# Optimization experiments

Hardware: AMD Instinct MI355X
Metric: run time of the kernel (lower is better)

The kernel has to match this reference:

```python
import jax, jax.numpy as jnp
import numpy as np
from jax import lax

B_, H_, W_, C_ = 2, 64, 64, 96
DI, N_, R_, K_ = 192, 16, 6, 4  # d_inner=expand*C, d_state, dt_rank=ceil(96/16), 4 scan dirs


def _ln(x, g, b, eps):
    m = jnp.mean(x, axis=-1, keepdims=True)
    v = jnp.var(x, axis=-1, keepdims=True)
    return (x - m) / jnp.sqrt(v + eps) * g + b


def _conv1x1(x, w, b=None):
    y = jnp.einsum('bihw,oi->bohw', x, w)
    return y if b is None else y + b[None, :, None, None]


def _dwconv(x, w):
    return lax.conv_general_dilated(x, w, (1, 1), 'SAME',
                                    feature_group_count=x.shape[1],
                                    dimension_numbers=('NCHW', 'OIHW', 'NCHW'))


def _ss2d(x, in_proj_w, conv2d_w, conv2d_b, x_proj_w, dt_proj_w, dt_proj_b,
          A_logs, Ds, out_norm_g, out_norm_b, out_proj_w):
    B, H, W, C = x.shape
    L = H * W
    xz = jnp.einsum('bhwc,dc->bhwd', x, in_proj_w)          # [B,H,W,2*DI]
    xx, z = jnp.split(xz, 2, axis=-1)
    xc = jnp.transpose(xx, (0, 3, 1, 2))                    # [B,DI,H,W]
    xc = jax.nn.silu(_dwconv(xc, conv2d_w) + conv2d_b[None, :, None, None])
    # 4 scan directions: row-major, col-major, and their reverses
    x_hwwh = jnp.stack([xc.reshape(B, DI, L),
                        jnp.transpose(xc, (0, 1, 3, 2)).reshape(B, DI, L)], axis=1)
    xs = jnp.concatenate([x_hwwh, jnp.flip(x_hwwh, axis=-1)], axis=1)  # [B,K,DI,L]
    x_dbl = jnp.einsum('bkdl,kcd->bkcl', xs, x_proj_w)
    dts, Bs, Cs = jnp.split(x_dbl, [R_, R_ + N_], axis=2)   # [B,K,R,L],[B,K,N,L],[B,K,N,L]
    dt = jnp.einsum('bkrl,kdr->bkdl', dts, dt_proj_w) + dt_proj_b[None, :, :, None]
    dt = jax.nn.softplus(dt)
    A = -jnp.exp(A_logs).reshape(K_, DI, N_)

    def step(h, inp):
        u_t, dt_t, B_t, C_t = inp                            # [B,K,DI],[B,K,DI],[B,K,N],[B,K,N]
        dA = jnp.exp(dt_t[..., None] * A)                    # [B,K,DI,N]
        h = h * dA + (dt_t * u_t)[..., None] * B_t[:, :, None, :]
        y = jnp.einsum('bkdn,bkn->bkd', h, C_t)
        return h, y

    inps = (jnp.moveaxis(xs, -1, 0), jnp.moveaxis(dt, -1, 0),
            jnp.moveaxis(Bs, -1, 0), jnp.moveaxis(Cs, -1, 0))
    h0 = jnp.zeros((B, K_, DI, N_), xs.dtype)
    _, ys = lax.scan(step, h0, inps)                         # [L,B,K,DI]
    out_y = jnp.moveaxis(ys, 0, -1) + xs * Ds.reshape(K_, DI)[None, :, :, None]
    inv = jnp.flip(out_y[:, 2:4], axis=-1)
    y1 = out_y[:, 0]
    y2 = inv[:, 0]
    y3 = jnp.transpose(out_y[:, 1].reshape(B, DI, W, H), (0, 1, 3, 2)).reshape(B, DI, L)
    y4 = jnp.transpose(inv[:, 1].reshape(B, DI, W, H), (0, 1, 3, 2)).reshape(B, DI, L)
    y = jnp.transpose(y1 + y2 + y3 + y4, (0, 2, 1)).reshape(B, H, W, DI)
    y = _ln(y, out_norm_g, out_norm_b, 1e-5)
    y = y * jax.nn.silu(z)
    return jnp.einsum('bhwd,cd->bhwc', y, out_proj_w)


def _fftm(x, f1_w, f1_b, fm_w, fm_b, f2_w, f2_b):
    x = jax.nn.silu(_conv1x1(x, f1_w, f1_b))                 # [B,C/2,H,W]
    f = jnp.fft.rfftn(x, axes=(-2, -1), norm='ortho')        # [B,C/2,H,W//2+1] complex
    B, Ch, Hh, Wf = f.shape
    fr = jnp.stack([f.real, f.imag], axis=2).reshape(B, 2 * Ch, Hh, Wf)
    fr = jax.nn.silu(_conv1x1(fr, fm_w, fm_b))
    fr = fr.reshape(B, Ch, 2, Hh, Wf)
    fc = lax.complex(fr[:, :, 0], fr[:, :, 1])
    out = jnp.fft.irfftn(fc, s=x.shape[-2:], axes=(-2, -1), norm='ortho')
    return _conv1x1(out, f2_w, f2_b)


def _mgcb(x, in_w, dw3_w, dw5_w, out_w, ca_w1, ca_b1, ca_w2, ca_b2):
    Hd = 2 * x.shape[1]                                      # hidden_features = 2*dim
    p = _conv1x1(x, in_w)                                    # [B,2*Hd,H,W]
    s1 = 3 * Hd // 2
    x1, x2 = p[:, :s1], p[:, s1:]
    d1 = _dwconv(x1, dw3_w)
    x1_1, x1_2 = d1[:, :Hd], d1[:, Hd:]
    x2 = _dwconv(x2, dw5_w)
    y = jax.nn.gelu(x1_1, approximate=False) * jnp.concatenate([x1_2, x2], axis=1)
    y = _conv1x1(y, out_w)
    a = jnp.mean(y, axis=(2, 3))                             # channel attention (squeeze 30)
    a = jax.nn.relu(a @ ca_w1.T + ca_b1)
    a = jax.nn.sigmoid(a @ ca_w2.T + ca_b2)
    return y * a[:, :, None, None]


def _forward(input, ln1_g, ln1_b, skip_scale, skip_scale2, ln2_g, ln2_b,
             in_proj_w, conv2d_w, conv2d_b, x_proj_w, dt_proj_w, dt_proj_b,
             A_logs, Ds, out_norm_g, out_norm_b, out_proj_w,
             f1_w, f1_b, fm_w, fm_b, f2_w, f2_b,
             mg_in_w, mg_dw3_w, mg_dw5_w, mg_out_w,
             ca_w1, ca_b1, ca_w2, ca_b2, h_size, w_size):
    B, L, C = input.shape
    x4 = input.reshape(B, h_size, w_size, C)
    xn = _ln(x4, ln1_g, ln1_b, 1e-6)
    attn = _ss2d(xn, in_proj_w, conv2d_w, conv2d_b, x_proj_w, dt_proj_w,
                 dt_proj_b, A_logs, Ds, out_norm_g, out_norm_b, out_proj_w)
    fft = _fftm(jnp.transpose(xn, (0, 3, 1, 2)), f1_w, f1_b, fm_w, fm_b, f2_w, f2_b)
    x = x4 * skip_scale + attn + jnp.transpose(fft, (0, 2, 3, 1))
    xn2 = _ln(x, ln2_g, ln2_b, 1e-5)
    conv = _mgcb(jnp.transpose(xn2, (0, 3, 1, 2)), mg_in_w, mg_dw3_w, mg_dw5_w,
                 mg_out_w, ca_w1, ca_b1, ca_w2, ca_b2)
    x = x * skip_scale2 + jnp.transpose(conv, (0, 2, 3, 1))
    return x.reshape(B, L, C)


def setup_inputs() -> dict:
    key = jax.random.key(0)
    ks = iter(jax.random.split(key, 48))
    def rn(shape, s=0.02):
        return jax.random.normal(next(ks), shape, jnp.float32) * s
    d = {}
    d['input'] = jax.random.normal(next(ks), (B_, H_ * W_, C_), jnp.float32)
    d['ln1_g'] = jnp.ones((C_,)); d['ln1_b'] = jnp.zeros((C_,))
    d['skip_scale'] = jnp.ones((C_,)); d['skip_scale2'] = jnp.ones((C_,))
    d['ln2_g'] = jnp.ones((C_,)); d['ln2_b'] = jnp.zeros((C_,))
    d['in_proj_w'] = rn((2 * DI, C_))
    d['conv2d_w'] = rn((DI, 1, 3, 3), 0.1); d['conv2d_b'] = jnp.zeros((DI,))
    d['x_proj_w'] = rn((K_, R_ + 2 * N_, DI))
    d['dt_proj_w'] = rn((K_, DI, R_), 0.1)
    d['dt_proj_b'] = jnp.full((K_, DI), -4.6, jnp.float32) + rn((K_, DI), 0.5)
    d['A_logs'] = jnp.log(jnp.tile(jnp.arange(1, N_ + 1, dtype=jnp.float32), (K_ * DI, 1)))
    d['Ds'] = jnp.ones((K_ * DI,))
    d['out_norm_g'] = jnp.ones((DI,)); d['out_norm_b'] = jnp.zeros((DI,))
    d['out_proj_w'] = rn((C_, DI))
    Ch = C_ // 2
    d['f1_w'] = rn((Ch, C_)); d['f1_b'] = jnp.zeros((Ch,))
    d['fm_w'] = rn((C_, C_)); d['fm_b'] = jnp.zeros((C_,))
    d['f2_w'] = rn((C_, Ch)); d['f2_b'] = jnp.zeros((C_,))
    Hd = 2 * C_
    d['mg_in_w'] = rn((2 * Hd, C_))
    d['mg_dw3_w'] = rn((3 * Hd // 2, 1, 3, 3), 0.1)
    d['mg_dw5_w'] = rn((Hd // 2, 1, 5, 5), 0.1)
    d['mg_out_w'] = rn((C_, Hd))
    Csq = C_ // 30
    d['ca_w1'] = rn((Csq, C_)); d['ca_b1'] = jnp.zeros((Csq,))
    d['ca_w2'] = rn((C_, Csq)); d['ca_b2'] = jnp.zeros((C_,))
    d['h_size'] = H_
    d['w_size'] = W_
    return d


def reference(input, ln1_g, ln1_b, skip_scale, skip_scale2, ln2_g, ln2_b,
              in_proj_w, conv2d_w, conv2d_b, x_proj_w, dt_proj_w, dt_proj_b,
              A_logs, Ds, out_norm_g, out_norm_b, out_proj_w,
              f1_w, f1_b, fm_w, fm_b, f2_w, f2_b,
              mg_in_w, mg_dw3_w, mg_dw5_w, mg_out_w,
              ca_w1, ca_b1, ca_w2, ca_b2, h_size, w_size):
    return _forward(input, ln1_g, ln1_b, skip_scale, skip_scale2, ln2_g, ln2_b,
                    in_proj_w, conv2d_w, conv2d_b, x_proj_w, dt_proj_w, dt_proj_b,
                    A_logs, Ds, out_norm_g, out_norm_b, out_proj_w,
                    f1_w, f1_b, fm_w, fm_b, f2_w, f2_b,
                    mg_in_w, mg_dw3_w, mg_dw5_w, mg_out_w,
                    ca_w1, ca_b1, ca_w2, ca_b2, h_size, w_size)
```

## Files before the change

kernel.cpp:

```cpp
#include <hip/hip_runtime.h>
#include <math.h>

#define DEV __device__ __forceinline__

constexpr int DI = 192, Nn = 16, Rr = 6;
constexpr int Cc = 96;
constexpr int Ll = 4096;
constexpr int NC = 64;

DEV float silu_(float x) { return x / (1.f + __expf(-x)); }
DEV float qadd1(float v) {
  int i = __builtin_amdgcn_mov_dpp(__float_as_int(v), 0xB1, 0xF, 0xF, true);
  return v + __int_as_float(i);
}
DEV float qadd2(float v) {
  int i = __builtin_amdgcn_mov_dpp(__float_as_int(v), 0x4E, 0xF, 0xF, true);
  return v + __int_as_float(i);
}

template<int CIN, int COUT, int CB, int PXB, int IN_MODE, int OUT_MODE, int ACT, int HAS_BIAS, int LN>
__global__ void conv1x1v2_kernel(const float* __restrict__ in, const float4* __restrict__ wt,
                                 const float* __restrict__ bias, float* __restrict__ out,
                                 float* __restrict__ out2, const float* __restrict__ lng,
                                 const float* __restrict__ lnb) {
  constexpr int J4 = CIN / 4, STR = J4 + 1, CCN = CB / 16, PXT = PXB / 16;
  constexpr int NPB = 8192 / PXB;
  __shared__ float4 xv[PXB * STR];
  int t = threadIdx.x;
  int pb = blockIdx.x % NPB;
  int cbase = (blockIdx.x / NPB) * CB;
  int pbase = pb * PXB;
  if (IN_MODE == 0) {
    for (int idx = t; idx < PXB * J4; idx += 256) {
      int px = idx / J4, j4 = idx - px * J4;
      xv[px * STR + j4] = ((const float4*)in)[(size_t)(pbase + px) * J4 + j4];
    }
  } else {
    for (int idx = t; idx < PXB * CIN; idx += 256) {
      int px = idx & (PXB - 1), c = idx / PXB;
      int gp = pbase + px; int b = gp >> 12, p = gp & 4095;
      ((float*)xv)[px * (STR * 4) + c] = in[((size_t)b * CIN + c) * Ll + p];
    }
  }
  __syncthreads();
  if constexpr (LN) {
    constexpr int TPX = 256 / PXB;
    constexpr int CHUNK = CIN / TPX;
    int px = t / TPX, sub = t % TPX;
    float* row = (float*)(xv + px * STR);
    float sm = 0.f, sq = 0.f;
    #pragma unroll
    for (int j2 = 0; j2 < CHUNK; ++j2) {
      float v = row[sub + j2 * TPX];
      sm += v; sq += v * v;
    }
    #pragma unroll
    for (int m = 1; m < TPX; m <<= 1) {
      sm += __shfl_xor(sm, m, 64);
      sq += __shfl_xor(sq, m, 64);
    }
    float mean = sm * (1.f / CIN);
    float rs = rsqrtf(sq * (1.f / CIN) - mean * mean + 1e-6f);
    #pragma unroll
    for (int j2 = 0; j2 < CHUNK; ++j2) {
      int j = sub + j2 * TPX;
      row[j] = (row[j] - mean) * rs * lng[j] + lnb[j];
    }
    __syncthreads();
  }
  int g = t >> 4, ci = t & 15;
  float acc[PXT][CCN];
  #pragma unroll
  for (int cc = 0; cc < CCN; ++cc) {
    float b0 = HAS_BIAS ? bias[cbase + ci + 16 * cc] : 0.f;
    #pragma unroll
    for (int p = 0; p < PXT; ++p) acc[p][cc] = b0;
  }
  #pragma unroll 2
  for (int j4 = 0; j4 < J4; ++j4) {
    float4 xr[PXT];
    #pragma unroll
    for (int p = 0; p < PXT; ++p) xr[p] = xv[(g + 16 * p) * STR + j4];
    #pragma unroll
    for (int cc = 0; cc < CCN; ++cc) {
      float4 w4 = wt[(size_t)j4 * COUT + cbase + ci + 16 * cc];
      #pragma unroll
      for (int p = 0; p < PXT; ++p)
        acc[p][cc] += xr[p].x * w4.x + xr[p].y * w4.y + xr[p].z * w4.z + xr[p].w * w4.w;
    }
  }
  #pragma unroll
  for (int p = 0; p < PXT; ++p) {
    int gp = pbase + g + 16 * p;
    #pragma unroll
    for (int cc = 0; cc < CCN; ++cc) {
      int c = cbase + ci + 16 * cc;
      float v = acc[p][cc];
      if (OUT_MODE == 2) {
        if (c < 192) out[(size_t)gp * 192 + c] = v;
        else out2[(size_t)gp * 192 + (c - 192)] = silu_(v);
      } else {
        if (ACT == 1) v = silu_(v);
        if (OUT_MODE == 0) out[(size_t)gp * COUT + c] = v;
        else { int bb = gp >> 12, p2 = gp & 4095; out[((size_t)bb * COUT + c) * Ll + p2] = v; }
      }
    }
  }
}

__global__ void outproj_fused_kernel(
    const float* __restrict__ outy, const float* __restrict__ zs,
    const float* __restrict__ ong, const float* __restrict__ onb,
    const float4* __restrict__ wt, const float* __restrict__ input,
    const float* __restrict__ fftout, const float* __restrict__ ss,
    const float* __restrict__ ln2g, const float* __restrict__ ln2b,
    float* __restrict__ xres, float* __restrict__ xn2) {
  __shared__ float4 xv[32 * 49];
  int t = threadIdx.x;
  int pbase = blockIdx.x * 32;
  {
    int px = t >> 3, sub = t & 7;
    int pix = pbase + px;
    int p = pix & 4095, b = pix >> 12;
    int pt = ((p & 63) << 6) | (p >> 6);
    size_t base = (size_t)b * 4 * Ll * DI;
    const float* y0 = outy + base + (size_t)p * DI;
    const float* y1 = outy + base + ((size_t)Ll + pt) * DI;
    const float* y2 = outy + base + ((size_t)2 * Ll + (4095 - p)) * DI;
    const float* y3 = outy + base + ((size_t)3 * Ll + (4095 - pt)) * DI;
    float v[24];
    float sm = 0.f, sq = 0.f;
    #pragma unroll
    for (int j = 0; j < 24; ++j) {
      int c = sub + 8 * j;
      float vv = y0[c] + y1[c] + y2[c] + y3[c];
      v[j] = vv; sm += vv; sq += vv * vv;
    }
    #pragma unroll
    for (int m = 1; m < 8; m <<= 1) {
      sm += __shfl_xor(sm, m, 64);
      sq += __shfl_xor(sq, m, 64);
    }
    float mean = sm * (1.f / 192.f);
    float rs = rsqrtf(sq * (1.f / 192.f) - mean * mean + 1e-5f);
    const float* zrow = zs + (size_t)pix * DI;
    float* row = (float*)(xv + px * 49);
    #pragma unroll
    for (int j = 0; j < 24; ++j) {
      int c = sub + 8 * j;
      row[c] = ((v[j] - mean) * rs * ong[c] + onb[c]) * zrow[c];
    }
  }
  __syncthreads();
  int g = t >> 4, ci = t & 15;
  float acc[2][6];
  #pragma unroll
  for (int pI = 0; pI < 2; ++pI)
    #pragma unroll
    for (int cc = 0; cc < 6; ++cc) acc[pI][cc] = 0.f;
  #pragma unroll 2
  for (int j4 = 0; j4 < 48; ++j4) {
    float4 xr0 = xv[g * 49 + j4];
    float4 xr1 = xv[(g + 16) * 49 + j4];
    #pragma unroll
    for (int cc = 0; cc < 6; ++cc) {
      float4 w4 = wt[(size_t)j4 * 96 + ci + 16 * cc];
      acc[0][cc] += xr0.x * w4.x + xr0.y * w4.y + xr0.z * w4.z + xr0.w * w4.w;
      acc[1][cc] += xr1.x * w4.x + xr1.y * w4.y + xr1.z * w4.z + xr1.w * w4.w;
    }
  }
  #pragma unroll
  for (int pI = 0; pI < 2; ++pI) {
    int gp = pbase + g + 16 * pI;
    float vv[6];
    float sm = 0.f, sq = 0.f;
    #pragma unroll
    for (int cc = 0; cc < 6; ++cc) {
      int c = ci + 16 * cc;
      float x = input[(size_t)gp * Cc + c] * ss[c] + acc[pI][cc] + fftout[(size_t)gp * Cc + c];
      vv[cc] = x; sm += x; sq += x * x;
    }
    #pragma unroll
    for (int m = 1; m < 16; m <<= 1) {
      sm += __shfl_xor(sm, m, 64);
      sq += __shfl_xor(sq, m, 64);
    }
    float mean = sm * (1.f / 96.f);
    float rs = rsqrtf(sq * (1.f / 96.f) - mean * mean + 1e-5f);
    #pragma unroll
    for (int cc = 0; cc < 6; ++cc) {
      int c = ci + 16 * cc;
      xres[(size_t)gp * Cc + c] = vv[cc];
      xn2[(size_t)gp * Cc + c] = (vv[cc] - mean) * rs * ln2g[c] + ln2b[c];
    }
  }
}

__global__ void mgout_fused_kernel(const float* __restrict__ in, const float4* __restrict__ wt,
                                   float* __restrict__ out, float* __restrict__ cap) {
  __shared__ float4 xv[32 * 49];
  __shared__ float redc[4][96];
  int t = threadIdx.x;
  int pbase = blockIdx.x * 32;
  for (int idx = t; idx < 32 * 48; idx += 256) {
    int px = idx / 48, j4 = idx - px * 48;
    xv[px * 49 + j4] = ((const float4*)in)[(size_t)(pbase + px) * 48 + j4];
  }
  __syncthreads();
  int g = t >> 4, ci = t & 15;
  float acc[2][6];
  #pragma unroll
  for (int pI = 0; pI < 2; ++pI)
    #pragma unroll
    for (int cc = 0; cc < 6; ++cc) acc[pI][cc] = 0.f;
  #pragma unroll 2
  for (int j4 = 0; j4 < 48; ++j4) {
    float4 xr0 = xv[g * 49 + j4];
    float4 xr1 = xv[(g + 16) * 49 + j4];
    #pragma unroll
    for (int cc = 0; cc < 6; ++cc) {
      float4 w4 = wt[(size_t)j4 * 96 + ci + 16 * cc];
      acc[0][cc] += xr0.x * w4.x + xr0.y * w4.y + xr0.z * w4.z + xr0.w * w4.w;
      acc[1][cc] += xr1.x * w4.x + xr1.y * w4.y + xr1.z * w4.z + xr1.w * w4.w;
    }
  }
  float ps[6];
  #pragma unroll
  for (int cc = 0; cc < 6; ++cc) ps[cc] = acc[0][cc] + acc[1][cc];
  #pragma unroll
  for (int pI = 0; pI < 2; ++pI) {
    int gp = pbase + g + 16 * pI;
    #pragma unroll
    for (int cc = 0; cc < 6; ++cc)
      out[(size_t)gp * 96 + ci + 16 * cc] = acc[pI][cc];
  }
  #pragma unroll
  for (int cc = 0; cc < 6; ++cc) {
    ps[cc] += __shfl_xor(ps[cc], 16, 64);
    ps[cc] += __shfl_xor(ps[cc], 32, 64);
  }
  if ((t & 63) < 16) {
    #pragma unroll
    for (int cc = 0; cc < 6; ++cc) redc[t >> 6][ci + 16 * cc] = ps[cc];
  }
  __syncthreads();
  if (t < 96)
    cap[(size_t)blockIdx.x * 96 + t] = redc[0][t] + redc[1][t] + redc[2][t] + redc[3][t];
}

__global__ void camerge_kernel(const float* __restrict__ cap, const float* __restrict__ w1,
                               const float* __restrict__ b1, const float* __restrict__ w2,
                               const float* __restrict__ b2, float* __restrict__ avec) {
  __shared__ float red[4][192];
  __shared__ float means[192];
  int t = threadIdx.x;
  int q = t / 192, r = t % 192;
  int b = r / 96, c = r % 96;
  float s = 0.f;
  for (int j = 0; j < 32; ++j)
    s += cap[(size_t)(b * 128 + q * 32 + j) * 96 + c];
  red[q][r] = s;
  __syncthreads();
  if (t < 192)
    means[t] = (red[0][t] + red[1][t] + red[2][t] + red[3][t]) * (1.f / 4096.f);
  __syncthreads();
  if (t < 192) {
    int bb = t / 96, cc2 = t % 96;
    float tt[3];
    #pragma unroll
    for (int j = 0; j < 3; ++j) {
      float a = b1[j];
      for (int cc = 0; cc < 96; ++cc) a += means[bb * 96 + cc] * w1[j * 96 + cc];
      tt[j] = fmaxf(a, 0.f);
    }
    float a2 = b2[cc2];
    #pragma unroll
    for (int j = 0; j < 3; ++j) a2 += tt[j] * w2[cc2 * 3 + j];
    avec[t] = 1.f / (1.f + expf(-a2));
  }
}

__global__ void wprep_all_kernel(const float* __restrict__ xpw, float4* __restrict__ xpwT,
                                 const float* __restrict__ cw, const float* __restrict__ mg3,
                                 const float* __restrict__ mg5, float* __restrict__ WC3T,
                                 float* __restrict__ W3T, float* __restrict__ W5T,
                                 const float* __restrict__ ipw, float4* __restrict__ WIPT,
                                 const float* __restrict__ mgiw, float4* __restrict__ WMGT,
                                 const float* __restrict__ opw, float4* __restrict__ WOPT,
                                 const float* __restrict__ mgow, float4* __restrict__ WMOT,
                                 const float* __restrict__ f1w, float4* __restrict__ WF1T,
                                 const float* __restrict__ f2w, float4* __restrict__ WF2T) {
  int idx = blockIdx.x * 256 + threadIdx.x;
  if (idx < 9216) {
    int k = idx / (48 * 48);
    int r = idx % (48 * 48);
    int j4 = r / 48, c = r % 48;
    float4 v = make_float4(0.f, 0.f, 0.f, 0.f);
    if (c < 38) v = ((const float4*)xpw)[((size_t)k * 38 + c) * 48 + j4];
    xpwT[((size_t)k * 48 + j4) * 48 + c] = v;
  }
  if (idx < 1728) { int c = idx / 9, j = idx % 9; WC3T[j * 192 + c] = cw[idx]; }
  if (idx < 2592) { int c = idx / 9, j = idx % 9; W3T[j * 288 + c] = mg3[idx]; }
  if (idx < 2400) { int c = idx / 25, j = idx % 25; W5T[j * 96 + c] = mg5[idx]; }
  if (idx < 9216) { int oc = idx % 384, j4 = idx / 384; WIPT[idx] = ((const float4*)ipw)[(size_t)oc * 24 + j4]; }
  if (idx < 9216) { int oc = idx % 384, j4 = idx / 384; WMGT[idx] = ((const float4*)mgiw)[(size_t)oc * 24 + j4]; }
  if (idx < 4608) { int oc = idx % 96, j4 = idx / 96; WOPT[idx] = ((const float4*)opw)[(size_t)oc * 48 + j4]; }
  if (idx < 4608) { int oc = idx % 96, j4 = idx / 96; WMOT[idx] = ((const float4*)mgow)[(size_t)oc * 48 + j4]; }
  if (idx < 1152) { int oc = idx % 48, j4 = idx / 48; WF1T[idx] = ((const float4*)f1w)[(size_t)oc * 24 + j4]; }
  if (idx < 1152) { int oc = idx % 96, j4 = idx / 96; WF2T[idx] = ((const float4*)f2w)[(size_t)oc * 12 + j4]; }
}

__global__ void dwconv3_silu_kernel(const float* __restrict__ xx, const float* __restrict__ wc3t,
                                    const float* __restrict__ bias, float* __restrict__ xc,
                                    float* __restrict__ xct) {
  int idx = blockIdx.x * 256 + threadIdx.x;
  int d4 = idx % 48;
  int p = (idx / 48) & (Ll - 1);
  int b = idx / (48 * Ll);
  int h = p >> 6, wq = p & 63;
  const float4* base = (const float4*)xx + (size_t)b * Ll * 48;
  const float4* wt = (const float4*)wc3t;
  float4 bv = ((const float4*)bias)[d4];
  float a0 = bv.x, a1 = bv.y, a2 = bv.z, a3 = bv.w;
  #pragma unroll
  for (int i = 0; i < 3; ++i) {
    int hh = h - 1 + i;
    if ((unsigned)hh >= 64u) continue;
    #pragma unroll
    for (int j = 0; j < 3; ++j) {
      int ww2 = wq - 1 + j;
      if ((unsigned)ww2 >= 64u) continue;
      float4 x = base[(size_t)(hh * 64 + ww2) * 48 + d4];
      float4 w4 = wt[(i * 3 + j) * 48 + d4];
      a0 += x.x * w4.x; a1 += x.y * w4.y; a2 += x.z * w4.z; a3 += x.w * w4.w;
    }
  }
  float4 v = make_float4(silu_(a0), silu_(a1), silu_(a2), silu_(a3));
  ((float4*)xc)[idx] = v;
  int pt = (wq << 6) | h;
  ((float4*)xct)[((size_t)b * Ll + pt) * 48 + d4] = v;
}

__global__ void proj_kernel(const float* __restrict__ xc, const float4* __restrict__ xpwT,
                            float* __restrict__ BSo, float* __restrict__ CSo,
                            float* __restrict__ DTS) {
  __shared__ float4 xv[32 * 49];
  int t = threadIdx.x;
  int pb = blockIdx.x & 127;
  int k = (blockIdx.x >> 7) & 3;
  int b = blockIdx.x >> 9;
  int bk = b * 4 + k;
  int pbase = pb * 32;
  for (int idx = t; idx < 32 * 48; idx += 256) {
    int it = idx / 48, j4 = idx - it * 48;
    xv[it * 49 + j4] = ((const float4*)xc)[((size_t)b * Ll + pbase + it) * 48 + j4];
  }
  __syncthreads();
  int g = t >> 4, ci = t & 15;
  float acc[2][3];
  #pragma unroll
  for (int p = 0; p < 2; ++p)
    #pragma unroll
    for (int cc = 0; cc < 3; ++cc) acc[p][cc] = 0.f;
  #pragma unroll 2
  for (int j4 = 0; j4 < 48; ++j4) {
    float4 xr0 = xv[g * 49 + j4];
    float4 xr1 = xv[(g + 16) * 49 + j4];
    const float4* wrow = xpwT + ((size_t)k * 48 + j4) * 48;
    #pragma unroll
    for (int cc = 0; cc < 3; ++cc) {
      float4 w4 = wrow[ci + 16 * cc];
      acc[0][cc] += xr0.x * w4.x + xr0.y * w4.y + xr0.z * w4.z + xr0.w * w4.w;
      acc[1][cc] += xr1.x * w4.x + xr1.y * w4.y + xr1.z * w4.z + xr1.w * w4.w;
    }
  }
  #pragma unroll
  for (int pI = 0; pI < 2; ++pI) {
    int p = pbase + g + 16 * pI;
    int pt = ((p & 63) << 6) | (p >> 6);
    int l = (k == 0) ? p : (k == 1) ? pt : (k == 2) ? (4095 - p) : (4095 - pt);
    #pragma unroll
    for (int cc = 0; cc < 3; ++cc) {
      int c = ci + 16 * cc;
      float v = acc[pI][cc];
      if (c < 6) DTS[((size_t)bk * 6 + c) * Ll + l] = v;
      else if (c < 22) BSo[((size_t)bk * Ll + l) * Nn + (c - 6)] = v;
      else if (c < 38) CSo[((size_t)bk * Ll + l) * Nn + (c - 22)] = v;
    }
  }
}

__global__ void dtproj_kernel(const float* __restrict__ dts, const float* __restrict__ dtw,
                              const float* __restrict__ dtb, float* __restrict__ DTo) {
  __shared__ float sdts[6][64];
  int t = threadIdx.x;
  int lb = (blockIdx.x & 63) * 64;
  int bk = blockIdx.x >> 6;
  int k = bk & 3;
  if (t < 384) {
    int r = t / 64, l = t & 63;
    sdts[r][l] = dts[((size_t)bk * 6 + r) * Ll + lb + l];
  }
  __syncthreads();
  int d = t;
  const float* wr = dtw + ((size_t)k * DI + d) * Rr;
  float w0 = wr[0], w1 = wr[1], w2 = wr[2], w3 = wr[3], w4 = wr[4], w5 = wr[5];
  float b0 = dtb[k * DI + d];
  float* ob = DTo + ((size_t)bk * Ll + lb) * DI + d;
  #pragma unroll 4
  for (int l = 0; l < 64; ++l) {
    float a = b0 + sdts[0][l] * w0 + sdts[1][l] * w1 + sdts[2][l] * w2
            + sdts[3][l] * w3 + sdts[4][l] * w4 + sdts[5][l] * w5;
    float sp = (a > 20.f) ? a : log1pf(__expf(a));
    ob[(size_t)l * DI] = sp;
  }
}

__global__ void scanA_kernel(const float* __restrict__ dtg, const float* __restrict__ xc,
                             const float* __restrict__ xct, const float* __restrict__ bsg,
                             const float* __restrict__ alog,
                             float* __restrict__ P, float* __restrict__ Q) {
  int g = blockIdx.x * 256 + threadIdx.x;
  int ng = g & 3;
  int t1 = g >> 2;
  int d = t1 % DI;
  int t2 = t1 / DI;
  int c = t2 & 63;
  int bk = t2 >> 6;
  int k = bk & 3, b = bk >> 2;
  float4 al = ((const float4*)alog)[(size_t)(k * DI + d) * 4 + ng];
  float An0 = -__expf(al.x), An1 = -__expf(al.y), An2 = -__expf(al.z), An3 = -__expf(al.w);
  const float* dtp = dtg + ((size_t)bk * Ll + c * 64) * DI + d;
  const float4* bsp = (const float4*)bsg + ((size_t)bk * Ll + c * 64) * 4 + ng;
  const float* usrc = (k & 1) ? xct : xc;
  int p0 = (k >= 2) ? (4095 - c * 64) : (c * 64);
  int ustep = (k >= 2) ? -DI : DI;
  const float* up = usrc + ((size_t)b * Ll + p0) * DI + d;
  float P0 = 1.f, P1 = 1.f, P2 = 1.f, P3 = 1.f;
  float Q0 = 0.f, Q1 = 0.f, Q2 = 0.f, Q3 = 0.f;
  float dpre[4], upre[4];
  float4 bpre[4];
  #pragma unroll
  for (int i = 0; i < 4; ++i) {
    dpre[i] = dtp[(size_t)i * DI];
    upre[i] = up[(ptrdiff_t)i * ustep];
    bpre[i] = bsp[(size_t)i * 4];
  }
  for (int tg = 0; tg < 64; tg += 4) {
    #pragma unroll
    for (int i = 0; i < 4; ++i) {
      float dtv = dpre[i], u = upre[i];
      float4 Bv = bpre[i];
      int tn = tg + 4 + i;
      dpre[i] = dtp[(size_t)tn * DI];
      upre[i] = up[(ptrdiff_t)tn * ustep];
      bpre[i] = bsp[(size_t)tn * 4];
      float s = dtv * u;
      float a0 = __expf(dtv * An0), a1 = __expf(dtv * An1);
      float a2 = __expf(dtv * An2), a3 = __expf(dtv * An3);
      P0 *= a0; P1 *= a1; P2 *= a2; P3 *= a3;
      Q0 = Q0 * a0 + s * Bv.x; Q1 = Q1 * a1 + s * Bv.y;
      Q2 = Q2 * a2 + s * Bv.z; Q3 = Q3 * a3 + s * Bv.w;
    }
  }
  ((float4*)P)[g] = make_float4(P0, P1, P2, P3);
  ((float4*)Q)[g] = make_float4(Q0, Q1, Q2, Q3);
}

__global__ void scanB_kernel(const float* __restrict__ P, const float* __restrict__ Q,
                             float* __restrict__ H0) {
  int g = blockIdx.x * 256 + threadIdx.x;
  int n = g & 15;
  int d = (g >> 4) % DI;
  int bk = (g >> 4) / DI;
  size_t base = (size_t)bk * NC * DI * Nn + (size_t)d * Nn + n;
  float Ppre[4], Qpre[4];
  #pragma unroll
  for (int i = 0; i < 4; ++i) {
    Ppre[i] = P[base + (size_t)i * 3072];
    Qpre[i] = Q[base + (size_t)i * 3072];
  }
  float h = 0.f;
  for (int cg = 0; cg < 64; cg += 4) {
    #pragma unroll
    for (int i = 0; i < 4; ++i) {
      float pv = Ppre[i], qv = Qpre[i];
      Ppre[i] = P[base + (size_t)(cg + 4 + i) * 3072];
      Qpre[i] = Q[base + (size_t)(cg + 4 + i) * 3072];
      H0[base + (size_t)(cg + i) * 3072] = h;
      h = pv * h + qv;
    }
  }
}

__global__ void scanC_kernel(const float* __restrict__ dtg, const float* __restrict__ xc,
                             const float* __restrict__ xct, const float* __restrict__ bsg,
                             const float* __restrict__ csg, const float* __restrict__ alog,
                             const float* __restrict__ Dsv_, const float* __restrict__ H0,
                             float* __restrict__ outy) {
  int g = blockIdx.x * 256 + threadIdx.x;
  int ng = g & 3;
  int t1 = g >> 2;
  int d = t1 % DI;
  int t2 = t1 / DI;
  int c = t2 & 63;
  int bk = t2 >> 6;
  int k = bk & 3, b = bk >> 2;
  float4 al = ((const float4*)alog)[(size_t)(k * DI + d) * 4 + ng];
  float An0 = -__expf(al.x), An1 = -__expf(al.y), An2 = -__expf(al.z), An3 = -__expf(al.w);
  float Dsv = Dsv_[k * DI + d];
  const float* dtp = dtg + ((size_t)bk * Ll + c * 64) * DI + d;
  const float4* bsp = (const float4*)bsg + ((size_t)bk * Ll + c * 64) * 4 + ng;
  const float4* csp = (const float4*)csg + ((size_t)bk * Ll + c * 64) * 4 + ng;
  const float* usrc = (k & 1) ? xct : xc;
  int p0 = (k >= 2) ? (4095 - c * 64) : (c * 64);
  int ustep = (k >= 2) ? -DI : DI;
  const float* up = usrc + ((size_t)b * Ll + p0) * DI + d;
  float* yo = outy + ((size_t)bk * Ll + c * 64) * DI + d;
  float4 h4 = ((const float4*)H0)[g];
  float h0 = h4.x, h1 = h4.y, h2 = h4.z, h3 = h4.w;
  float dpre[4], upre[4];
  float4 bpre[4], cpre[4];
  #pragma unroll
  for (int i = 0; i < 4; ++i) {
    dpre[i] = dtp[(size_t)i * DI];
    upre[i] = up[(ptrdiff_t)i * ustep];
    bpre[i] = bsp[(size_t)i * 4];
    cpre[i] = csp[(size_t)i * 4];
  }
  for (int tg = 0; tg < 64; tg += 4) {
    #pragma unroll
    for (int i = 0; i < 4; ++i) {
      float dtv = dpre[i], u = upre[i];
      float4 Bv = bpre[i], Cv = cpre[i];
      int tn = tg + 4 + i;
      dpre[i] = dtp[(size_t)tn * DI];
      upre[i] = up[(ptrdiff_t)tn * ustep];
      bpre[i] = bsp[(size_t)tn * 4];
      cpre[i] = csp[(size_t)tn * 4];
      float s = dtv * u;
      float a0 = __expf(dtv * An0), a1 = __expf(dtv * An1);
      float a2 = __expf(dtv * An2), a3 = __expf(dtv * An3);
      h0 = h0 * a0 + s * Bv.x; h1 = h1 * a1 + s * Bv.y;
      h2 = h2 * a2 + s * Bv.z; h3 = h3 * a3 + s * Bv.w;
      float yp = h0 * Cv.x + h1 * Cv.y + h2 * Cv.z + h3 * Cv.w;
      yp = qadd1(yp);
      yp = qadd2(yp);
      if (ng == 0) yo[(size_t)(tg + i) * DI] = yp + u * Dsv;
    }
  }
}

__global__ void dft_row_kernel(const float* __restrict__ xf, float* __restrict__ Tr,
                               float* __restrict__ Ti) {
  __shared__ float row[4][64];
  __shared__ float cs[64], sn[64];
  int t = threadIdx.x, lane = t & 63, wv = t >> 6;
  int bch = blockIdx.x * 4 + wv;
  int h = bch & 63, bc = bch >> 6;
  row[wv][lane] = xf[(size_t)bch * 64 + lane];
  if (t < 64) {
    float ang = (float)t * 0.09817477042468103f;
    float s0, c0; sincosf(ang, &s0, &c0); sn[t] = s0; cs[t] = c0;
  }
  __syncthreads();
  if (lane < 33) {
    float ar = 0.f, ai = 0.f;
    for (int wq = 0; wq < 64; ++wq) {
      int j = (lane * wq) & 63;
      ar += row[wv][wq] * cs[j];
      ai -= row[wv][wq] * sn[j];
    }
    Tr[((size_t)bc * 33 + lane) * 64 + h] = ar;
    Ti[((size_t)bc * 33 + lane) * 64 + h] = ai;
  }
}

__global__ void dft_col_kernel(const float* __restrict__ Tr, const float* __restrict__ Ti,
                               float* __restrict__ Gr, float* __restrict__ Gi) {
  __shared__ float tr[4][64], ti[4][64];
  __shared__ float cs[64], sn[64];
  int t = threadIdx.x, lane = t & 63, wv = t >> 6;
  int idx = blockIdx.x * 4 + wv;
  int v = idx % 33, bc = idx / 33;
  tr[wv][lane] = Tr[((size_t)bc * 33 + v) * 64 + lane];
  ti[wv][lane] = Ti[((size_t)bc * 33 + v) * 64 + lane];
  if (t < 64) {
    float ang = (float)t * 0.09817477042468103f;
    float s0, c0; sincosf(ang, &s0, &c0); sn[t] = s0; cs[t] = c0;
  }
  __syncthreads();
  float ar = 0.f, ai = 0.f;
  for (int hh = 0; hh < 64; ++hh) {
    int j = (lane * hh) & 63;
    ar += tr[wv][hh] * cs[j] + ti[wv][hh] * sn[j];
    ai += ti[wv][hh] * cs[j] - tr[wv][hh] * sn[j];
  }
  Gr[((size_t)bc * 64 + lane) * 33 + v] = ar * (1.f / 64.f);
  Gi[((size_t)bc * 64 + lane) * 33 + v] = ai * (1.f / 64.f);
}

__global__ void fmix2_kernel(const float* __restrict__ Gr, const float* __restrict__ Gi,
                             const float* __restrict__ w, const float* __restrict__ bias,
                             float* __restrict__ Mr, float* __restrict__ Mi) {
  __shared__ float xs[16][100];
  int t = threadIdx.x;
  int uvb = (blockIdx.x % 132) * 16;
  int b = blockIdx.x / 132;
  for (int idx = t; idx < 96 * 16; idx += 256) {
    int ch = idx >> 4, px = idx & 15;
    const float* src = (ch & 1) ? Gi : Gr;
    xs[px][ch] = src[((size_t)(b * 48 + (ch >> 1))) * 2112 + uvb + px];
  }
  __syncthreads();
  int px = t >> 4, ci = t & 15;
  float acc[6];
  #pragma unroll
  for (int cc = 0; cc < 6; ++cc) acc[cc] = bias[ci + 16 * cc];
  const float4* xr4 = (const float4*)&xs[px][0];
  #pragma unroll 2
  for (int j4 = 0; j4 < 24; ++j4) {
    float4 x4 = xr4[j4];
    #pragma unroll
    for (int cc = 0; cc < 6; ++cc) {
      float4 w4 = ((const float4*)w)[(size_t)(ci + 16 * cc) * 24 + j4];
      acc[cc] += x4.x * w4.x + x4.y * w4.y + x4.z * w4.z + x4.w * w4.w;
    }
  }
  int uv = uvb + px;
  int u = uv / 33, vv2 = uv % 33;
  #pragma unroll
  for (int cc = 0; cc < 6; ++cc) {
    int o = ci + 16 * cc;
    float v = silu_(acc[cc]);
    float* dst = (o & 1) ? Mi : Mr;
    dst[((size_t)(b * 48 + (o >> 1))) * 2112 + vv2 * 64 + u] = v;
  }
}

__global__ void idft_col_kernel(const float* __restrict__ Mr, const float* __restrict__ Mi,
                                float* __restrict__ gr, float* __restrict__ gi) {
  __shared__ float mr[4][64], mi[4][64];
  __shared__ float cs[64], sn[64];
  int t = threadIdx.x, lane = t & 63, wv = t >> 6;
  int idx = blockIdx.x * 4 + wv;
  int v = idx % 33, bc = idx / 33;
  mr[wv][lane] = Mr[((size_t)bc * 33 + v) * 64 + lane];
  mi[wv][lane] = Mi[((size_t)bc * 33 + v) * 64 + lane];
  if (t < 64) {
    float ang = (float)t * 0.09817477042468103f;
    float s0, c0; sincosf(ang, &s0, &c0); sn[t] = s0; cs[t] = c0;
  }
  __syncthreads();
  float ar = 0.f, ai = 0.f;
  for (int u = 0; u < 64; ++u) {
    int j = (lane * u) & 63;
    ar += mr[wv][u] * cs[j] - mi[wv][u] * sn[j];
    ai += mr[wv][u] * sn[j] + mi[wv][u] * cs[j];
  }
  gr[((size_t)bc * 64 + lane) * 33 + v] = ar;
  gi[((size_t)bc * 64 + lane) * 33 + v] = ai;
}

__global__ void irfft_row_kernel(const float* __restrict__ gr, const float* __restrict__ gi,
                                 float* __restrict__ ysp) {
  __shared__ float r[4][33], im[4][33];
  __shared__ float cs[64], sn[64];
  int t = threadIdx.x, lane = t & 63, wv = t >> 6;
  int bch = blockIdx.x * 4 + wv;
  if (lane < 33) {
    r[wv][lane] = gr[(size_t)bch * 33 + lane];
    im[wv][lane] = gi[(size_t)bch * 33 + lane];
  }
  if (t < 64) {
    float ang = (float)t * 0.09817477042468103f;
    float s0, c0; sincosf(ang, &s0, &c0); sn[t] = s0; cs[t] = c0;
  }
  __syncthreads();
  float acc = r[wv][0] + ((lane & 1) ? -r[wv][32] : r[wv][32]);
  for (int v = 1; v < 32; ++v) {
    int j = (v * lane) & 63;
    acc += 2.f * (r[wv][v] * cs[j] - im[wv][v] * sn[j]);
  }
  ysp[(size_t)bch * 64 + lane] = acc * (1.f / 64.f);
}

__global__ void mgcb_dw_kernel(const float* __restrict__ pm, const float* __restrict__ w3t,
                               const float* __restrict__ w5t, float* __restrict__ ymg) {
  int idx = blockIdx.x * 256 + threadIdx.x;
  int c4 = idx % 48;
  int p = (idx / 48) & (Ll - 1);
  int b = idx / (48 * Ll);
  int h = p >> 6, wq = p & 63;
  const float4* base = (const float4*)pm + (size_t)b * Ll * 96;
  const float4* wt3 = (const float4*)w3t;
  float g0 = 0.f, g1 = 0.f, g2 = 0.f, g3 = 0.f;
  float m0 = 0.f, m1 = 0.f, m2 = 0.f, m3 = 0.f;
  if (c4 < 24) {
    #pragma unroll
    for (int i = 0; i < 3; ++i) {
      int hh = h - 1 + i; if ((unsigned)hh >= 64u) continue;
      #pragma unroll
      for (int j = 0; j < 3; ++j) {
        int ww2 = wq - 1 + j; if ((unsigned)ww2 >= 64u) continue;
        const float4* px = base + (size_t)(hh * 64 + ww2) * 96;
        float4 xg = px[c4];
        float4 wg = wt3[(i * 3 + j) * 72 + c4];
        g0 += xg.x * wg.x; g1 += xg.y * wg.y; g2 += xg.z * wg.z; g3 += xg.w * wg.w;
        float4 xm = px[48 + c4];
        float4 wm = wt3[(i * 3 + j) * 72 + 48 + c4];
        m0 += xm.x * wm.x; m1 += xm.y * wm.y; m2 += xm.z * wm.z; m3 += xm.w * wm.w;
      }
    }
  } else {
    #pragma unroll
    for (int i = 0; i < 3; ++i) {
      int hh = h - 1 + i; if ((unsigned)hh >= 64u) continue;
      #pragma unroll
      for (int j = 0; j < 3; ++j) {
        int ww2 = wq - 1 + j; if ((unsigned)ww2 >= 64u) continue;
        float4 xg = base[(size_t)(hh * 64 + ww2) * 96 + c4];
        float4 wg = wt3[(i * 3 + j) * 72 + c4];
        g0 += xg.x * wg.x; g1 += xg.y * wg.y; g2 += xg.z * wg.z; g3 += xg.w * wg.w;
      }
    }
    const float4* wt5 = (const float4*)w5t;
    int cw4 = c4 - 24;
    #pragma unroll
    for (int i = 0; i < 5; ++i) {
      int hh = h - 2 + i; if ((unsigned)hh >= 64u) continue;
      #pragma unroll
      for (int j = 0; j < 5; ++j) {
        int ww2 = wq - 2 + j; if ((unsigned)ww2 >= 64u) continue;
        float4 xm = base[(size_t)(hh * 64 + ww2) * 96 + 48 + c4];
        float4 wm = wt5[(i * 5 + j) * 24 + cw4];
        m0 += xm.x * wm.x; m1 += xm.y * wm.y; m2 += xm.z * wm.z; m3 += xm.w * wm.w;
      }
    }
  }
  const float IS2 = 0.70710678118654752f;
  float4 o;
  o.x = 0.5f * g0 * (1.f + erff(g0 * IS2)) * m0;
  o.y = 0.5f * g1 * (1.f + erff(g1 * IS2)) * m1;
  o.z = 0.5f * g2 * (1.f + erff(g2 * IS2)) * m2;
  o.w = 0.5f * g3 * (1.f + erff(g3 * IS2)) * m3;
  ((float4*)ymg)[idx] = o;
}

__global__ void final_kernel(const float* __restrict__ xres, const float* __restrict__ yc,
                             const float* __restrict__ ss2, const float* __restrict__ avec,
                             float* __restrict__ out) {
  int i4 = blockIdx.x * 256 + threadIdx.x;
  int e0 = i4 * 4;
  int c = e0 % 96;
  int b = e0 / (Ll * 96);
  float4 xr = ((const float4*)xres)[i4];
  float4 yv = ((const float4*)yc)[i4];
  const float* av = avec + b * 96 + c;
  const float* sv = ss2 + c;
  float4 o;
  o.x = xr.x * sv[0] + yv.x * av[0];
  o.y = xr.y * sv[1] + yv.y * av[1];
  o.z = xr.z * sv[2] + yv.z * av[2];
  o.w = xr.w * sv[3] + yv.w * av[3];
  ((float4*)out)[i4] = o;
}

extern "C" void kernel_launch(void* const* d_in, const int* in_sizes, int n_in,
                              void* d_out, int out_size, void* d_ws, size_t ws_size,
                              hipStream_t stream) {
  const float* input      = (const float*)d_in[0];
  const float* ln1_g      = (const float*)d_in[1];
  const float* ln1_b      = (const float*)d_in[2];
  const float* skip_scale = (const float*)d_in[3];
  const float* skip_scale2= (const float*)d_in[4];
  const float* ln2_g      = (const float*)d_in[5];
  const float* ln2_b      = (const float*)d_in[6];
  const float* in_proj_w  = (const float*)d_in[7];
  const float* conv2d_w   = (const float*)d_in[8];
  const float* conv2d_b   = (const float*)d_in[9];
  const float* x_proj_w   = (const float*)d_in[10];
  const float* dt_proj_w  = (const float*)d_in[11];
  const float* dt_proj_b  = (const float*)d_in[12];
  const float* A_logs     = (const float*)d_in[13];
  const float* Ds         = (const float*)d_in[14];
  const float* out_norm_g = (const float*)d_in[15];
  const float* out_norm_b = (const float*)d_in[16];
  const float* out_proj_w = (const float*)d_in[17];
  const float* f1_w       = (const float*)d_in[18];
  const float* f1_b       = (const float*)d_in[19];
  const float* fm_w       = (const float*)d_in[20];
  const float* fm_b       = (const float*)d_in[21];
  const float* f2_w       = (const float*)d_in[22];
  const float* f2_b       = (const float*)d_in[23];
  const float* mg_in_w    = (const float*)d_in[24];
  const float* mg_dw3_w   = (const float*)d_in[25];
  const float* mg_dw5_w   = (const float*)d_in[26];
  const float* mg_out_w   = (const float*)d_in[27];
  const float* ca_w1      = (const float*)d_in[28];
  const float* ca_b1      = (const float*)d_in[29];
  const float* ca_w2      = (const float*)d_in[30];
  const float* ca_b2      = (const float*)d_in[31];

  float* W = (float*)d_ws;
  float* XN    = W;
  float* ZSILU = XN + 786432;
  float* XX    = ZSILU + 1572864;
  float* XC    = XX + 1572864;
  float* XCT   = XC + 1572864;
  float* DT    = XCT + 1572864;
  float* BSb   = DT + 6291456;
  float* CSb   = BSb + 524288;
  float* PP    = CSb + 524288;
  float* QQ    = PP + 1572864;
  float* H0    = QQ + 1572864;
  float* OUTY  = H0 + 1572864;
  float* YGATE = OUTY + 6291456;
  float* ATTN  = YGATE + 1572864;
  float* FFTOUT= ATTN + 786432;
  float* XRES  = FFTOUT + 786432;
  float* XN2   = XRES + 786432;
  float* MEANS = XN2 + 786432;
  float* AVEC  = MEANS + 192;
  float* XPWT  = AVEC + 192;
  float* WC3T  = XPWT + 36864;
  float* W3T   = WC3T + 1728;
  float* W5T   = W3T + 2592;
  float* CAP   = W5T + 2400;
  float* WIPT  = CAP + 24576;
  float* WMGT  = WIPT + 36864;
  float* WOPT  = WMGT + 36864;
  float* WMOT  = WOPT + 18432;
  float* WF1T  = WMOT + 18432;
  float* WF2T  = WF1T + 4608;
  float* DTS = H0;
  float* XF  = PP;
  float* TR  = XF + 393216;
  float* TI  = TR + 202752;
  float* GR  = TI + 202752;
  float* GI  = GR + 202752;
  float* MR  = TR;
  float* MI  = TI;
  float* G2R = GR;
  float* G2I = GI;
  float* YSP = GI + 202752;
  float* PMG = DT;
  float* YMG = DT + 3145728;
  float* YCb = YMG + 1572864;

  wprep_all_kernel<<<36, 256, 0, stream>>>(
      x_proj_w, (float4*)XPWT, conv2d_w, mg_dw3_w, mg_dw5_w, WC3T, W3T, W5T,
      in_proj_w, (float4*)WIPT, mg_in_w, (float4*)WMGT, out_proj_w, (float4*)WOPT,
      mg_out_w, (float4*)WMOT, f1_w, (float4*)WF1T, f2_w, (float4*)WF2T);
  conv1x1v2_kernel<96, 384, 96, 64, 0, 2, 0, 0, 1><<<512, 256, 0, stream>>>(
      input, (const float4*)WIPT, nullptr, XX, ZSILU, ln1_g, ln1_b);
  dwconv3_silu_kernel<<<1536, 256, 0, stream>>>(XX, WC3T, conv2d_b, XC, XCT);
  proj_kernel<<<1024, 256, 0, stream>>>(XC, (const float4*)XPWT, BSb, CSb, DTS);
  dtproj_kernel<<<512, 192, 0, stream>>>(DTS, dt_proj_w, dt_proj_b, DT);
  scanA_kernel<<<1536, 256, 0, stream>>>(DT, XC, XCT, BSb, A_logs, PP, QQ);
  scanB_kernel<<<96, 256, 0, stream>>>(PP, QQ, H0);
  conv1x1v2_kernel<96, 48, 48, 32, 0, 1, 1, 1, 1><<<256, 256, 0, stream>>>(
      input, (const float4*)WF1T, f1_b, XF, nullptr, ln1_g, ln1_b);
  dft_row_kernel<<<1536, 256, 0, stream>>>(XF, TR, TI);
  dft_col_kernel<<<792, 256, 0, stream>>>(TR, TI, GR, GI);
  fmix2_kernel<<<264, 256, 0, stream>>>(GR, GI, fm_w, fm_b, MR, MI);
  idft_col_kernel<<<792, 256, 0, stream>>>(MR, MI, G2R, G2I);
  irfft_row_kernel<<<1536, 256, 0, stream>>>(G2R, G2I, YSP);
  conv1x1v2_kernel<48, 96, 96, 32, 1, 0, 0, 1, 0><<<256, 256, 0, stream>>>(
      YSP, (const float4*)WF2T, f2_b, FFTOUT, nullptr, nullptr, nullptr);
  scanC_kernel<<<1536, 256, 0, stream>>>(DT, XC, XCT, BSb, CSb, A_logs, Ds, H0, OUTY);
  outproj_fused_kernel<<<256, 256, 0, stream>>>(
      OUTY, ZSILU, out_norm_g, out_norm_b, (const float4*)WOPT, input, FFTOUT,
      skip_scale, ln2_g, ln2_b, XRES, XN2);
  conv1x1v2_kernel<96, 384, 96, 64, 0, 0, 0, 0, 0><<<512, 256, 0, stream>>>(
      XN2, (const float4*)WMGT, nullptr, PMG, nullptr, nullptr, nullptr);
  mgcb_dw_kernel<<<1536, 256, 0, stream>>>(PMG, W3T, W5T, YMG);
  mgout_fused_kernel<<<256, 256, 0, stream>>>(YMG, (const float4*)WMOT, YCb, CAP);
  camerge_kernel<<<1, 768, 0, stream>>>(CAP, ca_w1, ca_b1, ca_w2, ca_b2, AVEC);
  final_kernel<<<768, 256, 0, stream>>>(XRES, YCb, skip_scale2, AVEC, (float*)d_out);
}
```

Baseline: 346.5 us.

## Fuse row and column DFT passes into per-channel 2D DFT kernels

The separate row-DFT and column-DFT kernels, and likewise the inverse column and row kernels, are merged so that one block per (batch, channel) plane does both passes through shared memory. This drops the global intermediate arrays and two kernel launches. The cost is that each fused kernel launches only 96 blocks, which may leave most compute units idle, and each block now carries far more serial work per thread using a naive O(N^2) DFT.

```diff
diff --git a/kernel.cpp b/kernel.cpp
--- a/kernel.cpp
+++ b/kernel.cpp
@@ -551,53 +551,45 @@
   }
 }
 
-__global__ void dft_row_kernel(const float* __restrict__ xf, float* __restrict__ Tr,
-                               float* __restrict__ Ti) {
-  __shared__ float row[4][64];
+__global__ void dft2d_kernel(const float* __restrict__ xf, float* __restrict__ Gr,
+                             float* __restrict__ Gi) {
+  __shared__ float xs[64][65];
+  __shared__ float tr[33][65], ti[33][65];
   __shared__ float cs[64], sn[64];
-  int t = threadIdx.x, lane = t & 63, wv = t >> 6;
-  int bch = blockIdx.x * 4 + wv;
-  int h = bch & 63, bc = bch >> 6;
-  row[wv][lane] = xf[(size_t)bch * 64 + lane];
+  int t = threadIdx.x;
+  int bc = blockIdx.x;
+  const float* src = xf + (size_t)bc * 4096;
+  for (int i = t; i < 4096; i += 256) xs[i >> 6][i & 63] = src[i];
   if (t < 64) {
     float ang = (float)t * 0.09817477042468103f;
     float s0, c0; sincosf(ang, &s0, &c0); sn[t] = s0; cs[t] = c0;
   }
   __syncthreads();
-  if (lane < 33) {
+  for (int o = t; o < 33 * 64; o += 256) {
+    int v = o >> 6, h = o & 63;
     float ar = 0.f, ai = 0.f;
-    for (int wq = 0; wq < 64; ++wq) {
-      int j = (lane * wq) & 63;
-      ar += row[wv][wq] * cs[j];
-      ai -= row[wv][wq] * sn[j];
-    }
-    Tr[((size_t)bc * 33 + lane) * 64 + h] = ar;
-    Ti[((size_t)bc * 33 + lane) * 64 + h] = ai;
-  }
-}
-
-__global__ void dft_col_kernel(const float* __restrict__ Tr, const float* __restrict__ Ti,
-                               float* __restrict__ Gr, float* __restrict__ Gi) {
-  __shared__ float tr[4][64], ti[4][64];
-  __shared__ float cs[64], sn[64];
-  int t = threadIdx.x, lane = t & 63, wv = t >> 6;
-  int idx = blockIdx.x * 4 + wv;
-  int v = idx % 33, bc = idx / 33;
-  tr[wv][lane] = Tr[((size_t)bc * 33 + v) * 64 + lane];
-  ti[wv][lane] = Ti[((size_t)bc * 33 + v) * 64 + lane];
-  if (t < 64) {
-    float ang = (float)t * 0.09817477042468103f;
-    float s0, c0; sincosf(ang, &s0, &c0); sn[t] = s0; cs[t] = c0;
-  }
-  __syncthreads();
-  float ar = 0.f, ai = 0.f;
-  for (int hh = 0; hh < 64; ++hh) {
-    int j = (lane * hh) & 63;
-    ar += tr[wv][hh] * cs[j] + ti[wv][hh] * sn[j];
-    ai += ti[wv][hh] * cs[j] - tr[wv][hh] * sn[j];
-  }
-  Gr[((size_t)bc * 64 + lane) * 33 + v] = ar * (1.f / 64.f);
-  Gi[((size_t)bc * 64 + lane) * 33 + v] = ai * (1.f / 64.f);
+    for (int w = 0; w < 64; ++w) {
+      int j = (v * w) & 63;
+      float x = xs[h][w];
+      ar += x * cs[j];
+      ai -= x * sn[j];
+    }
+    tr[v][h] = ar; ti[v][h] = ai;
+  }
+  __syncthreads();
+  for (int o = t; o < 64 * 33; o += 256) {
+    int u = o / 33, v = o - u * 33;
+    float ar = 0.f, ai = 0.f;
+    for (int h = 0; h < 64; ++h) {
+      int j = (u * h) & 63;
+      float c = cs[j], s = sn[j];
+      float trv = tr[v][h], tiv = ti[v][h];
+      ar += trv * c + tiv * s;
+      ai += tiv * c - trv * s;
+    }
+    Gr[((size_t)bc * 64 + u) * 33 + v] = ar * (1.f / 64.f);
+    Gi[((size_t)bc * 64 + u) * 33 + v] = ai * (1.f / 64.f);
+  }
 }
 
 __global__ void fmix2_kernel(const float* __restrict__ Gr, const float* __restrict__ Gi,
@@ -638,51 +630,47 @@
   }
 }
 
-__global__ void idft_col_kernel(const float* __restrict__ Mr, const float* __restrict__ Mi,
-                                float* __restrict__ gr, float* __restrict__ gi) {
-  __shared__ float mr[4][64], mi[4][64];
+__global__ void idft2d_kernel(const float* __restrict__ Mr, const float* __restrict__ Mi,
+                              float* __restrict__ ysp) {
+  __shared__ float mr[33][65], mi[33][65];
+  __shared__ float gr_[64][33], gi_[64][33];
   __shared__ float cs[64], sn[64];
-  int t = threadIdx.x, lane = t & 63, wv = t >> 6;
-  int idx = blockIdx.x * 4 + wv;
-  int v = idx % 33, bc = idx / 33;
-  mr[wv][lane] = Mr[((size_t)bc * 33 + v) * 64 + lane];
-  mi[wv][lane] = Mi[((size_t)bc * 33 + v) * 64 + lane];
+  int t = threadIdx.x;
+  int bc = blockIdx.x;
+  const float* srcR = Mr + (size_t)bc * 2112;
+  const float* srcI = Mi + (size_t)bc * 2112;
+  for (int i = t; i < 2112; i += 256) {
+    int v = i >> 6, u = i & 63;
+    mr[v][u] = srcR[i];
+    mi[v][u] = srcI[i];
+  }
   if (t < 64) {
     float ang = (float)t * 0.09817477042468103f;
     float s0, c0; sincosf(ang, &s0, &c0); sn[t] = s0; cs[t] = c0;
   }
   __syncthreads();
-  float ar = 0.f, ai = 0.f;
-  for (int u = 0; u < 64; ++u) {
-    int j = (lane * u) & 63;
-    ar += mr[wv][u] * cs[j] - mi[wv][u] * sn[j];
-    ai += mr[wv][u] * sn[j] + mi[wv][u] * cs[j];
-  }
-  gr[((size_t)bc * 64 + lane) * 33 + v] = ar;
-  gi[((size_t)bc * 64 + lane) * 33 + v] = ai;
-}
-
-__global__ void irfft_row_kernel(const float* __restrict__ gr, const float* __restrict__ gi,
-                                 float* __restrict__ ysp) {
-  __shared__ float r[4][33], im[4][33];
-  __shared__ float cs[64], sn[64];
-  int t = threadIdx.x, lane = t & 63, wv = t >> 6;
-  int bch = blockIdx.x * 4 + wv;
-  if (lane < 33) {
-    r[wv][lane] = gr[(size_t)bch * 33 + lane];
-    im[wv][lane] = gi[(size_t)bch * 33 + lane];
-  }
-  if (t < 64) {
-    float ang = (float)t * 0.09817477042468103f;
-    float s0, c0; sincosf(ang, &s0, &c0); sn[t] = s0; cs[t] = c0;
-  }
-  __syncthreads();
-  float acc = r[wv][0] + ((lane & 1) ? -r[wv][32] : r[wv][32]);
-  for (int v = 1; v < 32; ++v) {
-    int j = (v * lane) & 63;
-    acc += 2.f * (r[wv][v] * cs[j] - im[wv][v] * sn[j]);
-  }
-  ysp[(size_t)bch * 64 + lane] = acc * (1.f / 64.f);
+  for (int o = t; o < 64 * 33; o += 256) {
+    int h = o / 33, v = o - h * 33;
+    float ar = 0.f, ai = 0.f;
+    for (int u = 0; u < 64; ++u) {
+      int j = (h * u) & 63;
+      float c = cs[j], s = sn[j];
+      float r = mr[v][u], im = mi[v][u];
+      ar += r * c - im * s;
+      ai += r * s + im * c;
+    }
+    gr_[h][v] = ar; gi_[h][v] = ai;
+  }
+  __syncthreads();
+  for (int o = t; o < 4096; o += 256) {
+    int h = o >> 6, w = o & 63;
+    float acc = gr_[h][0] + ((w & 1) ? -gr_[h][32] : gr_[h][32]);
+    for (int v = 1; v < 32; ++v) {
+      int j = (v * w) & 63;
+      acc += 2.f * (gr_[h][v] * cs[j] - gi_[h][v] * sn[j]);
+    }
+    ysp[(size_t)bc * 4096 + o] = acc * (1.f / 64.f);
+  }
 }
 
 __global__ void mgcb_dw_kernel(const float* __restrict__ pm, const float* __restrict__ w3t,
@@ -841,8 +829,6 @@
   float* GI  = GR + 202752;
   float* MR  = TR;
   float* MI  = TI;
-  float* G2R = GR;
-  float* G2I = GI;
   float* YSP = GI + 202752;
   float* PMG = DT;
   float* YMG = DT + 3145728;
@@ -861,11 +847,9 @@
   scanB_kernel<<<96, 256, 0, stream>>>(PP, QQ, H0);
   conv1x1v2_kernel<96, 48, 48, 32, 0, 1, 1, 1, 1><<<256, 256, 0, stream>>>(
       input, (const float4*)WF1T, f1_b, XF, nullptr, ln1_g, ln1_b);
-  dft_row_kernel<<<1536, 256, 0, stream>>>(XF, TR, TI);
-  dft_col_kernel<<<792, 256, 0, stream>>>(TR, TI, GR, GI);
+  dft2d_kernel<<<96, 256, 0, stream>>>(XF, GR, GI);
   fmix2_kernel<<<264, 256, 0, stream>>>(GR, GI, fm_w, fm_b, MR, MI);
-  idft_col_kernel<<<792, 256, 0, stream>>>(MR, MI, G2R, G2I);
-  irfft_row_kernel<<<1536, 256, 0, stream>>>(G2R, G2I, YSP);
+  idft2d_kernel<<<96, 256, 0, stream>>>(MR, MI, YSP);
   conv1x1v2_kernel<48, 96, 96, 32, 1, 0, 0, 1, 0><<<256, 256, 0, stream>>>(
       YSP, (const float4*)WF2T, f2_b, FFTOUT, nullptr, nullptr, nullptr);
   scanC_kernel<<<1536, 256, 0, stream>>>(DT, XC, XCT, BSb, CSb, A_logs, Ds, H0, OUTY);
```

Result: slower. 401.9 us (+16.0%).
